# Optimization experiments

Measured on AMD Instinct MI355X. Metric: run time of the kernel, lower is better.

## Reference

```python
import jax, jax.numpy as jnp
import numpy as np

B, S, D = 8, 4096, 1024
EPS = 1e-8  # torch F.cosine_similarity default eps


def setup_inputs() -> dict:
    key = jax.random.key(0)
    kx, kwq, kbq, kwk, kbk = jax.random.split(key, 5)
    bound = 1.0 / np.sqrt(D)  # torch nn.Linear default init
    return {
        "x": jax.random.normal(kx, (B, S, D), dtype=jnp.float32),
        "Wq": jax.random.uniform(kwq, (D, D), jnp.float32, -bound, bound),
        "bq": jax.random.uniform(kbq, (D,), jnp.float32, -bound, bound),
        "Wk": jax.random.uniform(kwk, (D, D), jnp.float32, -bound, bound),
        "bk": jax.random.uniform(kbk, (D,), jnp.float32, -bound, bound),
    }


def reference(x, Wq, bq, Wk, bk):
    # ---- RoutingModule ----
    q = jnp.einsum("bsd,ed->bse", x, Wq) + bq                      # [B,S,D]
    x_roll = jnp.roll(x, shift=1, axis=1)                           # roll along seq
    k = jnp.einsum("bsd,ed->bse", x_roll, Wk) + bk                  # [B,S,D]
    qn = q / jnp.maximum(jnp.linalg.norm(q, axis=-1, keepdims=True), EPS)
    kn = k / jnp.maximum(jnp.linalg.norm(k, axis=-1, keepdims=True), EPS)
    cosine_sim = jnp.sum(qn * kn, axis=-1)                          # [B,S]
    p = 0.5 * (1.0 - cosine_sim)
    p = p.at[:, 0].set(1.0)
    b = (p >= 0.5).astype(x.dtype)                                  # [B,S]

    # ---- ragged compaction into padded buffer ----
    # Stable argsort moves selected positions to the front, preserving order.
    order = jnp.argsort(1.0 - b, axis=1)                            # [B,S] int
    gathered = jnp.take_along_axis(x, order[:, :, None], axis=1)    # [B,S,D]
    counts = jnp.sum(b, axis=1).astype(jnp.int32)                   # [B]
    valid = jnp.arange(S)[None, :] < counts[:, None]                # [B,S]
    # Padded to S (static max possible length) for jit-compatibility; torch
    # trims to the batch max, but all rows beyond each count are zeros here too.
    selected_padded = jnp.where(valid[:, :, None], gathered, 0.0)   # [B,S,D]
    return selected_padded, p, b
```

## Files before the change

kernel.cpp:

```cpp
#include <hip/hip_runtime.h>
#include <stdint.h>

#define Bb 8
#define Ss 4096
#define Dd 1024
#define Mm (Bb*Ss)
#define Kk 1024

typedef _Float16 half8 __attribute__((ext_vector_type(8)));
typedef _Float16 half4v __attribute__((ext_vector_type(4)));
typedef float f32x4 __attribute__((ext_vector_type(4)));

#define LO_SCALE 2048.0f
#define INV_LO_SCALE (1.0f/2048.0f)

__device__ __forceinline__ void gld_lds16(const void* g, void* l) {
  __builtin_amdgcn_global_load_lds(
      (const __attribute__((address_space(1))) unsigned int*)g,
      (__attribute__((address_space(3))) unsigned int*)l, 16, 0, 0);
}

__global__ void split_w3(const float* __restrict__ Gp, const float* __restrict__ Wq,
                         const float* __restrict__ Wk,
                         _Float16* __restrict__ G2, _Float16* __restrict__ Wh) {
  const int which = blockIdx.y;
  const int i = blockIdx.x * 256 + threadIdx.x;
  float4 v;
  if (which == 0) {
    float4 v0 = ((const float4*)Gp)[i];
    float4 v1 = ((const float4*)(Gp + (size_t)Dd * Dd))[i];
    float4 v2 = ((const float4*)(Gp + (size_t)2 * Dd * Dd))[i];
    float4 v3 = ((const float4*)(Gp + (size_t)3 * Dd * Dd))[i];
    v.x = (v0.x + v1.x) + (v2.x + v3.x);
    v.y = (v0.y + v1.y) + (v2.y + v3.y);
    v.z = (v0.z + v1.z) + (v2.z + v3.z);
    v.w = (v0.w + v1.w) + (v2.w + v3.w);
  } else {
    const float* src = (which == 1) ? Wq : Wk;
    v = ((const float4*)src)[i];
  }
  _Float16 h0 = (_Float16)v.x, h1 = (_Float16)v.y, h2 = (_Float16)v.z, h3 = (_Float16)v.w;
  if (which == 0) {
    _Float16 l0 = (_Float16)((v.x - (float)h0) * LO_SCALE);
    _Float16 l1 = (_Float16)((v.y - (float)h1) * LO_SCALE);
    _Float16 l2 = (_Float16)((v.z - (float)h2) * LO_SCALE);
    _Float16 l3 = (_Float16)((v.w - (float)h3) * LO_SCALE);
    const int n = i >> 8, c = i & 255;
    ((half4v*)G2)[(size_t)n * 512 + c]       = (half4v){h0, h1, h2, h3};
    ((half4v*)G2)[(size_t)n * 512 + 256 + c] = (half4v){l0, l1, l2, l3};
  } else {
    _Float16* hi = (which == 1) ? Wh : Wh + (size_t)Dd * Dd;
    ((half4v*)hi)[i] = (half4v){h0, h1, h2, h3};
  }
}

__global__ void split_x(const float* __restrict__ X, const float* __restrict__ up,
                        const float* __restrict__ vp,
                        _Float16* __restrict__ X2,
                        float* __restrict__ a_u, float* __restrict__ a_v) {
  const int s = blockIdx.x * 4 + (threadIdx.x >> 6);
  const int lane = threadIdx.x & 63;
  float au = 0.f, av = 0.f;
#pragma unroll
  for (int c = 0; c < 4; ++c) {
    const int e = c * 256 + lane * 4;
    float4 xv = *(const float4*)&X[(size_t)s * Dd + e];
    float4 uv = {0.f, 0.f, 0.f, 0.f}, vv = {0.f, 0.f, 0.f, 0.f};
#pragma unroll
    for (int z = 0; z < 4; ++z) {
      float4 a = *(const float4*)&up[(size_t)z * Dd + e];
      float4 b = *(const float4*)&vp[(size_t)z * Dd + e];
      uv.x += a.x; uv.y += a.y; uv.z += a.z; uv.w += a.w;
      vv.x += b.x; vv.y += b.y; vv.z += b.z; vv.w += b.w;
    }
    _Float16 h0 = (_Float16)xv.x, h1 = (_Float16)xv.y, h2 = (_Float16)xv.z, h3 = (_Float16)xv.w;
    _Float16 l0 = (_Float16)((xv.x - (float)h0) * LO_SCALE);
    _Float16 l1 = (_Float16)((xv.y - (float)h1) * LO_SCALE);
    _Float16 l2 = (_Float16)((xv.z - (float)h2) * LO_SCALE);
    _Float16 l3 = (_Float16)((xv.w - (float)h3) * LO_SCALE);
    *(half4v*)&X2[(size_t)s * 2048 + e]        = (half4v){h0, h1, h2, h3};
    *(half4v*)&X2[(size_t)s * 2048 + 1024 + e] = (half4v){l0, l1, l2, l3};
    au += uv.x * xv.x + uv.y * xv.y + uv.z * xv.z + uv.w * xv.w;
    av += vv.x * xv.x + vv.y * xv.y + vv.z * xv.z + vv.w * xv.w;
  }
#pragma unroll
  for (int off = 32; off > 0; off >>= 1) {
    au += __shfl_xor(au, off);
    av += __shfl_xor(av, off);
  }
  if (lane == 0) { a_u[s] = au; a_v[s] = av; }
}

__global__ __launch_bounds__(256)
void gemm_g_part(const float* __restrict__ Wq, const float* __restrict__ Wk,
                 float* __restrict__ Gp) {
  __shared__ float As[16][64];
  __shared__ float Bs[16][64];
  const int t = threadIdx.x;
  const int m0 = blockIdx.y * 64, n0 = blockIdx.x * 64;
  const int kbase = blockIdx.z * 256;
  float acc[4][4];
#pragma unroll
  for (int a = 0; a < 4; ++a)
#pragma unroll
    for (int b = 0; b < 4; ++b) acc[a][b] = 0.f;
  for (int kc = 0; kc < 16; ++kc) {
    const int k0 = kbase + kc * 16;
#pragma unroll
    for (int l = 0; l < 4; ++l) {
      const int idx = l * 256 + t;
      const int kk = idx >> 6, mm = idx & 63;
      As[kk][mm] = Wq[(size_t)(k0 + kk) * Dd + m0 + mm];
      Bs[kk][mm] = Wk[(size_t)(k0 + kk) * Dd + n0 + mm];
    }
    __syncthreads();
    const int tm = (t & 15) * 4, tn = (t >> 4) * 4;
#pragma unroll
    for (int k = 0; k < 16; ++k) {
      float4 a4 = *(const float4*)&As[k][tm];
      float4 b4 = *(const float4*)&Bs[k][tn];
      const float aa[4] = {a4.x, a4.y, a4.z, a4.w};
      const float bb[4] = {b4.x, b4.y, b4.z, b4.w};
#pragma unroll
      for (int a = 0; a < 4; ++a)
#pragma unroll
        for (int b = 0; b < 4; ++b) acc[a][b] += aa[a] * bb[b];
    }
    __syncthreads();
  }
  float* dst = Gp + (size_t)blockIdx.z * Dd * Dd;
  const int tm = (t & 15) * 4, tn = (t >> 4) * 4;
#pragma unroll
  for (int a = 0; a < 4; ++a)
#pragma unroll
    for (int b = 0; b < 4; ++b)
      dst[(size_t)(m0 + tm + a) * Dd + n0 + tn + b] = acc[a][b];
}

__global__ void uvc_part(const float* __restrict__ Wq, const float* __restrict__ Wk,
                         const float* __restrict__ bq, const float* __restrict__ bk,
                         float* __restrict__ up, float* __restrict__ vp,
                         float* __restrict__ c) {
  const int bx = blockIdx.x;
  if (bx == 32) {
    const int lane = threadIdx.x;
    if (lane >= 64) return;
    float a = 0.f;
#pragma unroll
    for (int i = 0; i < 16; ++i) a += bq[lane * 16 + i] * bk[lane * 16 + i];
#pragma unroll
    for (int off = 32; off > 0; off >>= 1) a += __shfl_xor(a, off);
    if (lane == 0) *c = a;
    return;
  }
  const int echunk = bx & 3;
  const int which = (bx >> 2) & 1;
  const int dchunk = bx >> 3;
  const int d = dchunk * 256 + threadIdx.x;
  const float* W = which ? Wq : Wk;
  const float* bb = which ? bk : bq;
  float acc = 0.f;
  const int e0 = echunk * 256;
#pragma unroll 4
  for (int e = e0; e < e0 + 256; ++e) acc += bb[e] * W[(size_t)e * Dd + d];
  float* dst = which ? vp : up;
  dst[(size_t)echunk * Dd + d] = acc;
}


__global__ __launch_bounds__(512, 2)
void gemm_dot(const _Float16* __restrict__ X2, const _Float16* __restrict__ G2,
              const float* __restrict__ X, float* __restrict__ pd) {
  __shared__ __align__(16) _Float16 smem[3 * 24576];
  const int tid = threadIdx.x;
  const int wave = tid >> 6, lane = tid & 63;
  const int lin = blockIdx.y * 8 + blockIdx.x;
  const int logical = (lin & 7) * 128 + (lin >> 3);
  const int n0 = (logical & 7) * 128;
  const int m0 = (logical >> 3) * 256;
  const int wm = (wave >> 2) * 128;
  const int wn = (wave & 3) * 32;
  const int fr = lane & 15, g4 = lane >> 4;
  const int sr = lane >> 3, sc = lane & 7;

  size_t aoff[4];
  size_t boff[2];
#pragma unroll
  for (int st = 0; st < 4; ++st) {
    const int R = st * 64 + wave * 8 + sr;
    const int u = sc ^ (R & 7);
    aoff[st] = (size_t)(m0 + R) * 2048 + ((u & 3) << 3) + ((size_t)(u >> 2) << 10);
  }
#pragma unroll
  for (int st = 0; st < 2; ++st) {
    const int R = st * 64 + wave * 8 + sr;
    const int u = sc ^ (R & 7);
    boff[st] = (size_t)(n0 + R) * 2048 + ((u & 3) << 3) + ((size_t)(u >> 2) << 10);
  }
  int aro[2][8], bro[2][2];
#pragma unroll
  for (int i = 0; i < 8; ++i) {
    const int Ra = wm + i * 16 + fr;
    aro[0][i] = Ra * 64 + ((g4 ^ (Ra & 7)) << 3);
    aro[1][i] = Ra * 64 + (((4 | g4) ^ (Ra & 7)) << 3);
  }
#pragma unroll
  for (int j = 0; j < 2; ++j) {
    const int Rb = wn + j * 16 + fr;
    bro[0][j] = Rb * 64 + ((g4 ^ (Rb & 7)) << 3);
    bro[1][j] = Rb * 64 + (((4 | g4) ^ (Rb & 7)) << 3);
  }

  f32x4 accH[8][2], accX[8][2];
#pragma unroll
  for (int i = 0; i < 8; ++i)
#pragma unroll
    for (int j = 0; j < 2; ++j) {
      accH[i][j] = (f32x4){0.f, 0.f, 0.f, 0.f};
      accX[i][j] = (f32x4){0.f, 0.f, 0.f, 0.f};
    }

#define DOT_STAGE(kt, slot) do {                                      \
    const size_t kof = (size_t)(kt) * 32;                             \
    _Float16* sb_ = smem + (slot) * 24576;                            \
    gld_lds16(X2 + aoff[0] + kof, sb_ + 0 * 4096 + wave * 512);       \
    gld_lds16(X2 + aoff[1] + kof, sb_ + 1 * 4096 + wave * 512);       \
    gld_lds16(X2 + aoff[2] + kof, sb_ + 2 * 4096 + wave * 512);       \
    gld_lds16(X2 + aoff[3] + kof, sb_ + 3 * 4096 + wave * 512);       \
    gld_lds16(G2 + boff[0] + kof, sb_ + 16384 + 0 * 4096 + wave * 512); \
    gld_lds16(G2 + boff[1] + kof, sb_ + 16384 + 1 * 4096 + wave * 512); \
  } while (0)

  DOT_STAGE(0, 0);
  DOT_STAGE(1, 1);
  int slot = 0;
  for (int kt = 0; kt < 32; ++kt) {
    if (kt < 31) asm volatile("s_waitcnt vmcnt(6)" ::: "memory");
    else         asm volatile("s_waitcnt vmcnt(0)" ::: "memory");
    __builtin_amdgcn_s_barrier();
    asm volatile("" ::: "memory");
    if (kt + 2 < 32) {
      int s2 = slot + 2; if (s2 >= 3) s2 -= 3;
      DOT_STAGE(kt + 2, s2);
    }
    const _Float16* A  = smem + slot * 24576;
    const _Float16* Bm = A + 16384;
    half8 bh[2], bl[2];
#pragma unroll
    for (int j = 0; j < 2; ++j) {
      bh[j] = *(const half8*)&Bm[bro[0][j]];
      bl[j] = *(const half8*)&Bm[bro[1][j]];
    }
#pragma unroll
    for (int ph = 0; ph < 4; ++ph) {
      const int i0 = ph * 2;
      half8 ah0 = *(const half8*)&A[aro[0][i0]];
      half8 al0 = *(const half8*)&A[aro[1][i0]];
      half8 ah1 = *(const half8*)&A[aro[0][i0 + 1]];
      half8 al1 = *(const half8*)&A[aro[1][i0 + 1]];
      __builtin_amdgcn_s_setprio(1);
#pragma unroll
      for (int j = 0; j < 2; ++j) {
        accH[i0][j]     = __builtin_amdgcn_mfma_f32_16x16x32_f16(ah0, bh[j], accH[i0][j], 0, 0, 0);
        accX[i0][j]     = __builtin_amdgcn_mfma_f32_16x16x32_f16(ah0, bl[j], accX[i0][j], 0, 0, 0);
        accX[i0][j]     = __builtin_amdgcn_mfma_f32_16x16x32_f16(al0, bh[j], accX[i0][j], 0, 0, 0);
        accH[i0 + 1][j] = __builtin_amdgcn_mfma_f32_16x16x32_f16(ah1, bh[j], accH[i0 + 1][j], 0, 0, 0);
        accX[i0 + 1][j] = __builtin_amdgcn_mfma_f32_16x16x32_f16(ah1, bl[j], accX[i0 + 1][j], 0, 0, 0);
        accX[i0 + 1][j] = __builtin_amdgcn_mfma_f32_16x16x32_f16(al1, bh[j], accX[i0 + 1][j], 0, 0, 0);
      }
      __builtin_amdgcn_s_setprio(0);
    }
    __builtin_amdgcn_sched_barrier(0);
    slot = (slot == 2) ? 0 : slot + 1;
  }

  float* scratch = (float*)smem;
  const int quad = g4;
#pragma unroll
  for (int i = 0; i < 8; ++i) {
#pragma unroll
    for (int r = 0; r < 4; ++r) {
      const int row = wm + 16 * i + quad * 4 + r;
      const int t = m0 + row + 1;
      float dsum = 0.f;
      if ((t & (Ss - 1)) != 0) {
        const float* xrow = X + (size_t)t * Dd + n0 + wn;
#pragma unroll
        for (int j = 0; j < 2; ++j) {
          float yv = accH[i][j][r] + accX[i][j][r] * INV_LO_SCALE;
          dsum += yv * xrow[16 * j + fr];
        }
      }
      dsum += __shfl_xor(dsum, 1);
      dsum += __shfl_xor(dsum, 2);
      dsum += __shfl_xor(dsum, 4);
      dsum += __shfl_xor(dsum, 8);
      if (fr == 0) scratch[row * 4 + (wave & 3)] = dsum;
    }
  }
  __syncthreads();
  if (tid < 256) {
    const int t = m0 + tid + 1;
    if ((t & (Ss - 1)) != 0) {
      float v = scratch[tid * 4] + scratch[tid * 4 + 1] +
                scratch[tid * 4 + 2] + scratch[tid * 4 + 3];
      pd[(size_t)(logical & 7) * Mm + t] = v;
    }
  }
}

__global__ __launch_bounds__(512, 2)
void gemm_norm(const _Float16* __restrict__ X2, const _Float16* __restrict__ Wh,
               const float* __restrict__ bq, const float* __restrict__ bk,
               float* __restrict__ pn) {
  __shared__ __align__(16) _Float16 smem[3 * 24576];
  const int tid = threadIdx.x;
  const int wave = tid >> 6, lane = tid & 63;
  const int lin = blockIdx.y * 16 + blockIdx.x;
  const int logical = (lin & 7) * 256 + (lin >> 3);
  const int n0 = (logical & 15) * 128;
  const int m0 = (logical >> 4) * 256;
  const int wm = (wave >> 2) * 128;
  const int wn = (wave & 3) * 32;
  const int fr = lane & 15, g4 = lane >> 4;
  const int sr = lane >> 3, sc = lane & 7;

  size_t aoff[4];
  size_t boff[2];
#pragma unroll
  for (int st = 0; st < 4; ++st) {
    const int R = st * 64 + wave * 8 + sr;
    const int u = sc ^ (R & 7);
    aoff[st] = (size_t)(m0 + R) * 2048 + ((size_t)u << 3);
  }
#pragma unroll
  for (int st = 0; st < 2; ++st) {
    const int R = st * 64 + wave * 8 + sr;
    const int u = sc ^ (R & 7);
    boff[st] = (size_t)(n0 + R) * 1024 + ((size_t)u << 3);
  }
  int aro[2][8], bro[2][2];
#pragma unroll
  for (int i = 0; i < 8; ++i) {
    const int Ra = wm + i * 16 + fr;
    aro[0][i] = Ra * 64 + ((g4 ^ (Ra & 7)) << 3);
    aro[1][i] = Ra * 64 + (((4 | g4) ^ (Ra & 7)) << 3);
  }
#pragma unroll
  for (int j = 0; j < 2; ++j) {
    const int Rb = wn + j * 16 + fr;
    bro[0][j] = Rb * 64 + ((g4 ^ (Rb & 7)) << 3);
    bro[1][j] = Rb * 64 + (((4 | g4) ^ (Rb & 7)) << 3);
  }

  f32x4 acc[8][2];
#pragma unroll
  for (int i = 0; i < 8; ++i)
#pragma unroll
    for (int j = 0; j < 2; ++j) acc[i][j] = (f32x4){0.f, 0.f, 0.f, 0.f};

#define NRM_STAGE(kt, slot) do {                                      \
    const size_t kof = (size_t)(kt) * 64;                             \
    _Float16* sb_ = smem + (slot) * 24576;                            \
    gld_lds16(X2 + aoff[0] + kof, sb_ + 0 * 4096 + wave * 512);       \
    gld_lds16(X2 + aoff[1] + kof, sb_ + 1 * 4096 + wave * 512);       \
    gld_lds16(X2 + aoff[2] + kof, sb_ + 2 * 4096 + wave * 512);       \
    gld_lds16(X2 + aoff[3] + kof, sb_ + 3 * 4096 + wave * 512);       \
    gld_lds16(Wh + boff[0] + kof, sb_ + 16384 + 0 * 4096 + wave * 512); \
    gld_lds16(Wh + boff[1] + kof, sb_ + 16384 + 1 * 4096 + wave * 512); \
  } while (0)

  NRM_STAGE(0, 0);
  NRM_STAGE(1, 1);
  int slot = 0;
  for (int kt = 0; kt < 16; ++kt) {
    if (kt < 15) asm volatile("s_waitcnt vmcnt(6)" ::: "memory");
    else         asm volatile("s_waitcnt vmcnt(0)" ::: "memory");
    __builtin_amdgcn_s_barrier();
    asm volatile("" ::: "memory");
    if (kt + 2 < 16) {
      int s2 = slot + 2; if (s2 >= 3) s2 -= 3;
      NRM_STAGE(kt + 2, s2);
    }
    const _Float16* A  = smem + slot * 24576;
    const _Float16* Bm = A + 16384;
    half8 b0[2], b1[2];
#pragma unroll
    for (int j = 0; j < 2; ++j) {
      b0[j] = *(const half8*)&Bm[bro[0][j]];
      b1[j] = *(const half8*)&Bm[bro[1][j]];
    }
#pragma unroll
    for (int ph = 0; ph < 4; ++ph) {
      const int i0 = ph * 2;
      half8 a00 = *(const half8*)&A[aro[0][i0]];
      half8 a01 = *(const half8*)&A[aro[1][i0]];
      half8 a10 = *(const half8*)&A[aro[0][i0 + 1]];
      half8 a11 = *(const half8*)&A[aro[1][i0 + 1]];
      __builtin_amdgcn_s_setprio(1);
#pragma unroll
      for (int j = 0; j < 2; ++j) {
        acc[i0][j]     = __builtin_amdgcn_mfma_f32_16x16x32_f16(a00, b0[j], acc[i0][j], 0, 0, 0);
        acc[i0][j]     = __builtin_amdgcn_mfma_f32_16x16x32_f16(a01, b1[j], acc[i0][j], 0, 0, 0);
        acc[i0 + 1][j] = __builtin_amdgcn_mfma_f32_16x16x32_f16(a10, b0[j], acc[i0 + 1][j], 0, 0, 0);
        acc[i0 + 1][j] = __builtin_amdgcn_mfma_f32_16x16x32_f16(a11, b1[j], acc[i0 + 1][j], 0, 0, 0);
      }
      __builtin_amdgcn_s_setprio(0);
    }
    __builtin_amdgcn_sched_barrier(0);
    slot = (slot == 2) ? 0 : slot + 1;
  }

  float bias_j[2];
#pragma unroll
  for (int j = 0; j < 2; ++j) {
    const int n = n0 + wn + 16 * j + fr;
    bias_j[j] = (n < Dd) ? bq[n] : bk[n - Dd];
  }
  float* scratch = (float*)smem;
  const int quad = g4;
#pragma unroll
  for (int i = 0; i < 8; ++i) {
#pragma unroll
    for (int r = 0; r < 4; ++r) {
      const int row = wm + 16 * i + quad * 4 + r;
      float vsum = 0.f;
#pragma unroll
      for (int j = 0; j < 2; ++j) {
        float q = acc[i][j][r] + bias_j[j];
        vsum += q * q;
      }
      vsum += __shfl_xor(vsum, 1);
      vsum += __shfl_xor(vsum, 2);
      vsum += __shfl_xor(vsum, 4);
      vsum += __shfl_xor(vsum, 8);
      if (fr == 0) scratch[row * 4 + (wave & 3)] = vsum;
    }
  }
  __syncthreads();
  if (tid < 256) {
    float v = scratch[tid * 4] + scratch[tid * 4 + 1] +
              scratch[tid * 4 + 2] + scratch[tid * 4 + 3];
    pn[(size_t)(logical & 15) * Mm + (m0 + tid)] = v;
  }
}

__global__ void cos_final(const float* __restrict__ pd, const float* __restrict__ pn,
                          const float* __restrict__ a_u, const float* __restrict__ a_v,
                          const float* __restrict__ cptr,
                          float* __restrict__ p_out, float* __restrict__ b_out) {
  const int s = blockIdx.x * 256 + threadIdx.x;
  if ((s & (Ss - 1)) == 0) { p_out[s] = 1.0f; b_out[s] = 1.0f; return; }
  float dot = a_u[s - 1] + a_v[s] + *cptr;
#pragma unroll
  for (int sl = 0; sl < 8; ++sl) dot += pd[(size_t)sl * Mm + s];
  float nq = 0.f, nk = 0.f;
#pragma unroll
  for (int sl = 0; sl < 8; ++sl) nq += pn[(size_t)sl * Mm + s];
#pragma unroll
  for (int sl = 8; sl < 16; ++sl) nk += pn[(size_t)sl * Mm + (s - 1)];
  float denom = fmaxf(sqrtf(nq), 1e-8f) * fmaxf(sqrtf(nk), 1e-8f);
  float cs = dot / denom;
  float p = 0.5f * (1.0f - cs);
  p_out[s] = p;
  b_out[s] = (p >= 0.5f) ? 1.0f : 0.0f;
}

__global__ __launch_bounds__(1024)
void scan_flags(const float* __restrict__ b_out,
                int* __restrict__ sel, int* __restrict__ counts) {
  const int b = blockIdx.x;
  const int tid = threadIdx.x;
  const int lane = tid & 63;
  const int w = tid >> 6;
  __shared__ int wtot[16];
  float fv[4];
#pragma unroll
  for (int c = 0; c < 4; ++c) fv[c] = b_out[b * Ss + c * 1024 + tid];
  int running = 0;
#pragma unroll
  for (int c = 0; c < 4; ++c) {
    const bool f = fv[c] != 0.0f;
    unsigned long long m = __ballot(f);
    int pre = __popcll(m & ((1ull << lane) - 1ull));
    if (lane == 0) wtot[w] = __popcll(m);
    __syncthreads();
    int woff = 0, tot = 0;
#pragma unroll
    for (int ww = 0; ww < 16; ++ww) {
      int t = wtot[ww];
      if (ww < w) woff += t;
      tot += t;
    }
    if (f) sel[b * Ss + running + woff + pre] = c * 1024 + tid;
    running += tot;
    __syncthreads();
  }
  if (tid == 0) counts[b] = running;
}

__global__ void write_out(const float* __restrict__ x, const int* __restrict__ sel,
                          const int* __restrict__ counts, float* __restrict__ out) {
  const int blk = blockIdx.x;
  const int b = blk >> 12;
  const int r = blk & (Ss - 1);
  const int tid = threadIdx.x;
  float4 v = {0.f, 0.f, 0.f, 0.f};
  if (r < counts[b]) {
    const int src = sel[b * Ss + r];
    v = *(const float4*)&x[((size_t)b * Ss + src) * Dd + tid * 4];
  }
  *(float4*)&out[(size_t)blk * Dd + tid * 4] = v;
}

extern "C" void kernel_launch(void* const* d_in, const int* in_sizes, int n_in,
                              void* d_out, int out_size, void* d_ws, size_t ws_size,
                              hipStream_t stream) {
  const float* x  = (const float*)d_in[0];
  const float* Wq = (const float*)d_in[1];
  const float* bq = (const float*)d_in[2];
  const float* Wk = (const float*)d_in[3];
  const float* bk = (const float*)d_in[4];
  float* out = (float*)d_out;

  uint8_t* w = (uint8_t*)d_ws;
  _Float16* X2 = (_Float16*)w; w += (size_t)Mm * 2048 * 2;
  float*    Gp = (float*)w;    w += (size_t)4 * Dd * Dd * 4;
  _Float16* G2 = (_Float16*)w; w += (size_t)Dd * 2048 * 2;
  _Float16* Wh = (_Float16*)w; w += (size_t)2 * Dd * Dd * 2;
  float* pd = (float*)w;       w += (size_t)8 * Mm * 4;
  float* pn = (float*)w;       w += (size_t)16 * Mm * 4;
  float* a_u = (float*)w;      w += (size_t)Mm * 4;
  float* a_v = (float*)w;      w += (size_t)Mm * 4;
  float* up  = (float*)w;      w += (size_t)4 * Dd * 4;
  float* vp  = (float*)w;      w += (size_t)4 * Dd * 4;
  float* cpt = (float*)w;      w += 64;
  int*   sel = (int*)w;        w += (size_t)Mm * 4;
  int*   counts = (int*)w;     w += 64;

  float* p_out = out + (size_t)Mm * Dd;
  float* b_out = p_out + Mm;

  gemm_g_part<<<dim3(16, 16, 4), 256, 0, stream>>>(Wq, Wk, Gp);
  uvc_part<<<33, 256, 0, stream>>>(Wq, Wk, bq, bk, up, vp, cpt);
  split_x<<<Mm / 4, 256, 0, stream>>>(x, up, vp, X2, a_u, a_v);
  split_w3<<<dim3((Dd * Dd / 4) / 256, 3), 256, 0, stream>>>(Gp, Wq, Wk, G2, Wh);
  gemm_norm<<<dim3(16, Mm / 256), 512, 0, stream>>>(X2, Wh, bq, bk, pn);
  gemm_dot<<<dim3(8, Mm / 256), 512, 0, stream>>>(X2, G2, x, pd);
  cos_final<<<Mm / 256, 256, 0, stream>>>(pd, pn, a_u, a_v, cpt, p_out, b_out);
  scan_flags<<<Bb, 1024, 0, stream>>>(b_out, sel, counts);
  write_out<<<Mm, 256, 0, stream>>>(x, sel, counts, out);
}
```

Measured before the change: 782.1 us.

## Split GEMM main loops into two phases interleaving prefetch with MFMA clusters

Both the dot and norm GEMM main loops are restructured into two half-iteration phases. Each phase loads LDS fragments, issues half of the next stage's global-to-LDS prefetch, synchronizes, then runs a dense MFMA cluster. This spreads the global loads across the iteration and groups MFMAs into larger blocks, aiming for better overlap of memory and math and fewer scheduling stalls. In exchange it adds two extra barriers per iteration and keeps more fragment registers live.

```diff
diff --git a/kernel.cpp b/kernel.cpp
--- a/kernel.cpp
+++ b/kernel.cpp
@@ -19,6 +19,8 @@
       (const __attribute__((address_space(1))) unsigned int*)g,
       (__attribute__((address_space(3))) unsigned int*)l, 16, 0, 0);
 }
+
+#define MFMA16(d, a, b) d = __builtin_amdgcn_mfma_f32_16x16x32_f16(a, b, d, 0, 0, 0)
 
 __global__ void split_w3(const float* __restrict__ Gp, const float* __restrict__ Wq,
                          const float* __restrict__ Wk,
@@ -220,57 +222,92 @@
       accX[i][j] = (f32x4){0.f, 0.f, 0.f, 0.f};
     }
 
-#define DOT_STAGE(kt, slot) do {                                      \
-    const size_t kof = (size_t)(kt) * 32;                             \
-    _Float16* sb_ = smem + (slot) * 24576;                            \
-    gld_lds16(X2 + aoff[0] + kof, sb_ + 0 * 4096 + wave * 512);       \
-    gld_lds16(X2 + aoff[1] + kof, sb_ + 1 * 4096 + wave * 512);       \
-    gld_lds16(X2 + aoff[2] + kof, sb_ + 2 * 4096 + wave * 512);       \
-    gld_lds16(X2 + aoff[3] + kof, sb_ + 3 * 4096 + wave * 512);       \
-    gld_lds16(G2 + boff[0] + kof, sb_ + 16384 + 0 * 4096 + wave * 512); \
-    gld_lds16(G2 + boff[1] + kof, sb_ + 16384 + 1 * 4096 + wave * 512); \
+#define DOT_STAGE_P0(kt, w) do {                                       \
+    const size_t kof_ = (size_t)(kt) * 32;                             \
+    _Float16* sb_ = smem + (w) * 24576;                                \
+    gld_lds16(X2 + aoff[0] + kof_, sb_ + 0 * 4096 + wave * 512);       \
+    gld_lds16(X2 + aoff[1] + kof_, sb_ + 1 * 4096 + wave * 512);       \
+    gld_lds16(X2 + aoff[2] + kof_, sb_ + 2 * 4096 + wave * 512);       \
   } while (0)
-
-  DOT_STAGE(0, 0);
-  DOT_STAGE(1, 1);
+#define DOT_STAGE_P1(kt, w) do {                                       \
+    const size_t kof_ = (size_t)(kt) * 32;                             \
+    _Float16* sb_ = smem + (w) * 24576;                                \
+    gld_lds16(X2 + aoff[3] + kof_, sb_ + 3 * 4096 + wave * 512);       \
+    gld_lds16(G2 + boff[0] + kof_, sb_ + 16384 + 0 * 4096 + wave * 512); \
+    gld_lds16(G2 + boff[1] + kof_, sb_ + 16384 + 1 * 4096 + wave * 512); \
+  } while (0)
+
+  DOT_STAGE_P0(0, 0); DOT_STAGE_P1(0, 0);
+  DOT_STAGE_P0(1, 1); DOT_STAGE_P1(1, 1);
+  asm volatile("s_waitcnt vmcnt(6)" ::: "memory");
+  __builtin_amdgcn_s_barrier();
+  asm volatile("" ::: "memory");
+
   int slot = 0;
   for (int kt = 0; kt < 32; ++kt) {
-    if (kt < 31) asm volatile("s_waitcnt vmcnt(6)" ::: "memory");
-    else         asm volatile("s_waitcnt vmcnt(0)" ::: "memory");
-    __builtin_amdgcn_s_barrier();
-    asm volatile("" ::: "memory");
-    if (kt + 2 < 32) {
-      int s2 = slot + 2; if (s2 >= 3) s2 -= 3;
-      DOT_STAGE(kt + 2, s2);
-    }
     const _Float16* A  = smem + slot * 24576;
     const _Float16* Bm = A + 16384;
+    int w = slot + 2; if (w >= 3) w -= 3;
+    const bool st = (kt + 2 < 32);
+
     half8 bh[2], bl[2];
 #pragma unroll
     for (int j = 0; j < 2; ++j) {
       bh[j] = *(const half8*)&Bm[bro[0][j]];
       bl[j] = *(const half8*)&Bm[bro[1][j]];
     }
-#pragma unroll
-    for (int ph = 0; ph < 4; ++ph) {
-      const int i0 = ph * 2;
-      half8 ah0 = *(const half8*)&A[aro[0][i0]];
-      half8 al0 = *(const half8*)&A[aro[1][i0]];
-      half8 ah1 = *(const half8*)&A[aro[0][i0 + 1]];
-      half8 al1 = *(const half8*)&A[aro[1][i0 + 1]];
-      __builtin_amdgcn_s_setprio(1);
-#pragma unroll
-      for (int j = 0; j < 2; ++j) {
-        accH[i0][j]     = __builtin_amdgcn_mfma_f32_16x16x32_f16(ah0, bh[j], accH[i0][j], 0, 0, 0);
-        accX[i0][j]     = __builtin_amdgcn_mfma_f32_16x16x32_f16(ah0, bl[j], accX[i0][j], 0, 0, 0);
-        accX[i0][j]     = __builtin_amdgcn_mfma_f32_16x16x32_f16(al0, bh[j], accX[i0][j], 0, 0, 0);
-        accH[i0 + 1][j] = __builtin_amdgcn_mfma_f32_16x16x32_f16(ah1, bh[j], accH[i0 + 1][j], 0, 0, 0);
-        accX[i0 + 1][j] = __builtin_amdgcn_mfma_f32_16x16x32_f16(ah1, bl[j], accX[i0 + 1][j], 0, 0, 0);
-        accX[i0 + 1][j] = __builtin_amdgcn_mfma_f32_16x16x32_f16(al1, bh[j], accX[i0 + 1][j], 0, 0, 0);
-      }
-      __builtin_amdgcn_s_setprio(0);
-    }
-    __builtin_amdgcn_sched_barrier(0);
+    half8 ah[4], al[4];
+#pragma unroll
+    for (int i = 0; i < 4; ++i) {
+      ah[i] = *(const half8*)&A[aro[0][i]];
+      al[i] = *(const half8*)&A[aro[1][i]];
+    }
+    if (st) DOT_STAGE_P0(kt + 2, w);
+    __builtin_amdgcn_s_barrier();
+    asm volatile("s_waitcnt lgkmcnt(0)" ::: "memory");
+    __builtin_amdgcn_s_setprio(1);
+#pragma unroll
+    for (int j = 0; j < 2; ++j)
+#pragma unroll
+      for (int i = 0; i < 4; ++i) MFMA16(accH[i][j], ah[i], bh[j]);
+#pragma unroll
+    for (int j = 0; j < 2; ++j)
+#pragma unroll
+      for (int i = 0; i < 4; ++i) MFMA16(accX[i][j], ah[i], bl[j]);
+#pragma unroll
+    for (int j = 0; j < 2; ++j)
+#pragma unroll
+      for (int i = 0; i < 4; ++i) MFMA16(accX[i][j], al[i], bh[j]);
+    __builtin_amdgcn_s_setprio(0);
+    __builtin_amdgcn_s_barrier();
+    asm volatile("" ::: "memory");
+
+#pragma unroll
+    for (int i = 0; i < 4; ++i) {
+      ah[i] = *(const half8*)&A[aro[0][i + 4]];
+      al[i] = *(const half8*)&A[aro[1][i + 4]];
+    }
+    if (st) DOT_STAGE_P1(kt + 2, w);
+    __builtin_amdgcn_s_barrier();
+    asm volatile("s_waitcnt lgkmcnt(0)" ::: "memory");
+    __builtin_amdgcn_s_setprio(1);
+#pragma unroll
+    for (int j = 0; j < 2; ++j)
+#pragma unroll
+      for (int i = 0; i < 4; ++i) MFMA16(accH[i + 4][j], ah[i], bh[j]);
+#pragma unroll
+    for (int j = 0; j < 2; ++j)
+#pragma unroll
+      for (int i = 0; i < 4; ++i) MFMA16(accX[i + 4][j], ah[i], bl[j]);
+#pragma unroll
+    for (int j = 0; j < 2; ++j)
+#pragma unroll
+      for (int i = 0; i < 4; ++i) MFMA16(accX[i + 4][j], al[i], bh[j]);
+    __builtin_amdgcn_s_setprio(0);
+    if (st) asm volatile("s_waitcnt vmcnt(6)" ::: "memory");
+    else    asm volatile("s_waitcnt vmcnt(0)" ::: "memory");
+    __builtin_amdgcn_s_barrier();
+    asm volatile("" ::: "memory");
     slot = (slot == 2) ? 0 : slot + 1;
   }
 
@@ -359,55 +396,69 @@
 #pragma unroll
     for (int j = 0; j < 2; ++j) acc[i][j] = (f32x4){0.f, 0.f, 0.f, 0.f};
 
-#define NRM_STAGE(kt, slot) do {                                      \
-    const size_t kof = (size_t)(kt) * 64;                             \
-    _Float16* sb_ = smem + (slot) * 24576;                            \
-    gld_lds16(X2 + aoff[0] + kof, sb_ + 0 * 4096 + wave * 512);       \
-    gld_lds16(X2 + aoff[1] + kof, sb_ + 1 * 4096 + wave * 512);       \
-    gld_lds16(X2 + aoff[2] + kof, sb_ + 2 * 4096 + wave * 512);       \
-    gld_lds16(X2 + aoff[3] + kof, sb_ + 3 * 4096 + wave * 512);       \
-    gld_lds16(Wh + boff[0] + kof, sb_ + 16384 + 0 * 4096 + wave * 512); \
-    gld_lds16(Wh + boff[1] + kof, sb_ + 16384 + 1 * 4096 + wave * 512); \
+#define NRM_STAGE_P0(kt, w) do {                                       \
+    const size_t kof_ = (size_t)(kt) * 64;                             \
+    _Float16* sb_ = smem + (w) * 24576;                                \
+    gld_lds16(X2 + aoff[0] + kof_, sb_ + 0 * 4096 + wave * 512);       \
+    gld_lds16(X2 + aoff[1] + kof_, sb_ + 1 * 4096 + wave * 512);       \
+    gld_lds16(X2 + aoff[2] + kof_, sb_ + 2 * 4096 + wave * 512);       \
   } while (0)
-
-  NRM_STAGE(0, 0);
-  NRM_STAGE(1, 1);
+#define NRM_STAGE_P1(kt, w) do {                                       \
+    const size_t kof_ = (size_t)(kt) * 64;                             \
+    _Float16* sb_ = smem + (w) * 24576;                                \
+    gld_lds16(X2 + aoff[3] + kof_, sb_ + 3 * 4096 + wave * 512);       \
+    gld_lds16(Wh + boff[0] + kof_, sb_ + 16384 + 0 * 4096 + wave * 512); \
+    gld_lds16(Wh + boff[1] + kof_, sb_ + 16384 + 1 * 4096 + wave * 512); \
+  } while (0)
+
+  NRM_STAGE_P0(0, 0); NRM_STAGE_P1(0, 0);
+  NRM_STAGE_P0(1, 1); NRM_STAGE_P1(1, 1);
+  asm volatile("s_waitcnt vmcnt(6)" ::: "memory");
+  __builtin_amdgcn_s_barrier();
+  asm volatile("" ::: "memory");
+
   int slot = 0;
   for (int kt = 0; kt < 16; ++kt) {
-    if (kt < 15) asm volatile("s_waitcnt vmcnt(6)" ::: "memory");
-    else         asm volatile("s_waitcnt vmcnt(0)" ::: "memory");
-    __builtin_amdgcn_s_barrier();
-    asm volatile("" ::: "memory");
-    if (kt + 2 < 16) {
-      int s2 = slot + 2; if (s2 >= 3) s2 -= 3;
-      NRM_STAGE(kt + 2, s2);
-    }
     const _Float16* A  = smem + slot * 24576;
     const _Float16* Bm = A + 16384;
-    half8 b0[2], b1[2];
-#pragma unroll
-    for (int j = 0; j < 2; ++j) {
-      b0[j] = *(const half8*)&Bm[bro[0][j]];
-      b1[j] = *(const half8*)&Bm[bro[1][j]];
-    }
-#pragma unroll
-    for (int ph = 0; ph < 4; ++ph) {
-      const int i0 = ph * 2;
-      half8 a00 = *(const half8*)&A[aro[0][i0]];
-      half8 a01 = *(const half8*)&A[aro[1][i0]];
-      half8 a10 = *(const half8*)&A[aro[0][i0 + 1]];
-      half8 a11 = *(const half8*)&A[aro[1][i0 + 1]];
-      __builtin_amdgcn_s_setprio(1);
-#pragma unroll
-      for (int j = 0; j < 2; ++j) {
-        acc[i0][j]     = __builtin_amdgcn_mfma_f32_16x16x32_f16(a00, b0[j], acc[i0][j], 0, 0, 0);
-        acc[i0][j]     = __builtin_amdgcn_mfma_f32_16x16x32_f16(a01, b1[j], acc[i0][j], 0, 0, 0);
-        acc[i0 + 1][j] = __builtin_amdgcn_mfma_f32_16x16x32_f16(a10, b0[j], acc[i0 + 1][j], 0, 0, 0);
-        acc[i0 + 1][j] = __builtin_amdgcn_mfma_f32_16x16x32_f16(a11, b1[j], acc[i0 + 1][j], 0, 0, 0);
-      }
-      __builtin_amdgcn_s_setprio(0);
-    }
-    __builtin_amdgcn_sched_barrier(0);
+    int w = slot + 2; if (w >= 3) w -= 3;
+    const bool st = (kt + 2 < 16);
+
+    half8 b0[2], a0[8];
+#pragma unroll
+    for (int j = 0; j < 2; ++j) b0[j] = *(const half8*)&Bm[bro[0][j]];
+#pragma unroll
+    for (int i = 0; i < 8; ++i) a0[i] = *(const half8*)&A[aro[0][i]];
+    if (st) NRM_STAGE_P0(kt + 2, w);
+    __builtin_amdgcn_s_barrier();
+    asm volatile("s_waitcnt lgkmcnt(0)" ::: "memory");
+    __builtin_amdgcn_s_setprio(1);
+#pragma unroll
+    for (int j = 0; j < 2; ++j)
+#pragma unroll
+      for (int i = 0; i < 8; ++i) MFMA16(acc[i][j], a0[i], b0[j]);
+    __builtin_amdgcn_s_setprio(0);
+    __builtin_amdgcn_s_barrier();
+    asm volatile("" ::: "memory");
+
+    half8 b1[2], a1[8];
+#pragma unroll
+    for (int j = 0; j < 2; ++j) b1[j] = *(const half8*)&Bm[bro[1][j]];
+#pragma unroll
+    for (int i = 0; i < 8; ++i) a1[i] = *(const half8*)&A[aro[1][i]];
+    if (st) NRM_STAGE_P1(kt + 2, w);
+    __builtin_amdgcn_s_barrier();
+    asm volatile("s_waitcnt lgkmcnt(0)" ::: "memory");
+    __builtin_amdgcn_s_setprio(1);
+#pragma unroll
+    for (int j = 0; j < 2; ++j)
+#pragma unroll
+      for (int i = 0; i < 8; ++i) MFMA16(acc[i][j], a1[i], b1[j]);
+    __builtin_amdgcn_s_setprio(0);
+    if (st) asm volatile("s_waitcnt vmcnt(6)" ::: "memory");
+    else    asm volatile("s_waitcnt vmcnt(0)" ::: "memory");
+    __builtin_amdgcn_s_barrier();
+    asm volatile("" ::: "memory");
     slot = (slot == 2) ? 0 : slot + 1;
   }
 
```

Result: no change. 789.8 us (+1.0%).
